# Performance work log

Hardware: AMD Instinct MI355X
Metric: run time of the kernel (lower is better)

## Reference

```python
import jax, jax.numpy as jnp
import numpy as np

NUM_HEADS = 8
H_NUM, W_NUM = 1, 2   # idx=0 stripe windows
SCALE = float((256 // NUM_HEADS) ** -0.5)  # qk_scale


def _partition(x, h_sp, w_sp):
    # x: (T,B,C,H,W) -> (T, B*nWin, heads, N, C//heads) with N = h_sp*w_sp
    T, B, C, H, W = x.shape
    x = x.reshape(T, B, C, H // h_sp, h_sp, W // w_sp, w_sp)
    x = x.transpose(0, 1, 3, 5, 4, 6, 2)  # T,B,nH,nW,h_sp,w_sp,C
    x = x.reshape(T, -1, h_sp * w_sp, NUM_HEADS, C // NUM_HEADS)
    return x.transpose(0, 1, 3, 2, 4)


def setup_inputs() -> dict:
    key = jax.random.key(0)
    k1, k2, k3 = jax.random.split(key, 3)
    shape = (4, 2, 256, 56, 56)
    return {
        "q": jax.random.normal(k1, shape, jnp.float32),
        "k": jax.random.normal(k2, shape, jnp.float32),
        "v": jax.random.normal(k3, shape, jnp.float32),
        "v_lamda": 1,
    }


def reference(q, k, v, v_lamda):
    T, B, C, H0, W0 = q.shape
    h_pad = (-H0) % H_NUM
    w_pad = (-W0) % W_NUM
    pad = ((0, 0), (0, 0), (0, 0), (0, h_pad), (0, w_pad))
    q = jnp.pad(q, pad)
    k = jnp.pad(k, pad)
    v = jnp.pad(v, pad)
    H, W = H0 + h_pad, W0 + w_pad
    h_sp, w_sp = H // H_NUM, W // W_NUM

    qw = _partition(q, h_sp, w_sp)  # (T, BnW, h, N, d)
    kw = _partition(k, h_sp, w_sp)
    vw = _partition(v, h_sp, w_sp)  # head dim = C*v_lamda//heads

    attn = jnp.einsum('twhnd,twhmd->twhnm', qw, kw)          # (QK^T), no softmax
    out = jnp.einsum('twhnm,twhmd->twhnd', attn, vw) * (SCALE * 2)

    # merge windows back: (T,BnW,h,N,d) -> (T,B,Cv,H,W)
    Cv = C * v_lamda
    out = out.transpose(0, 1, 3, 2, 4).reshape(T, -1, h_sp * w_sp, Cv)
    out = out.reshape(T, B, H_NUM, W_NUM, h_sp, w_sp, Cv)
    out = out.transpose(0, 1, 2, 4, 3, 5, 6).reshape(T, B, H, W, Cv)
    out = out.transpose(0, 1, 4, 2, 3)
    return out[:, :, :, :H0, :W0]
```

## Files before the change

### kernel.cpp

```cpp
#include <hip/hip_runtime.h>


#define HW 3136
#define WDIM 56
#define NPOS 1568
#define NPROB 128
#define SPLIT 14
#define PSPLIT 112
#define SCALE2 0.35355339059327373f

typedef const __attribute__((address_space(1))) void gas_void;
typedef __attribute__((address_space(3))) void las_void;

__global__ __launch_bounds__(256) void kv_kernel(const float* __restrict__ K,
                                                 const float* __restrict__ V,
                                                 float* __restrict__ Mpart) {
    __shared__ float lds[2 * 32 * PSPLIT];

    const int blk = blockIdx.x;
    const int p   = blk / SPLIT;
    const int s   = blk - p * SPLIT;
    const int head = p & 7;
    const int win  = (p >> 3) & 1;
    const int b    = (p >> 4) & 1;
    const int t    = p >> 5;

    const size_t base = (size_t)((t * 2 + b) * 256 + head * 32) * HW;
    const float* __restrict__ Kb = K + base;
    const float* __restrict__ Vb = V + base;

    const int tid = threadIdx.x;
    const int l   = tid & 63;
    const int w   = tid >> 6;

    #pragma unroll
    for (int i = 0; i < 7; ++i) {
        const int q   = (w * 7 + i) * 64 + l;
        const int isv = q >= 896 ? 1 : 0;
        const int r   = q - isv * 896;
        const int ch  = r / 28;
        const int pq  = r - ch * 28;
        const int n   = s * PSPLIT + pq * 4;
        const int y   = n / 28;
        const int x   = n - y * 28;
        const float* src = (isv ? Vb : Kb)
                         + (size_t)ch * HW + y * WDIM + win * 28 + x;
        float* dst = &lds[w * 1792 + i * 256];
        __builtin_amdgcn_global_load_lds((gas_void*)src, (las_void*)dst, 16, 0, 0);
    }
    __syncthreads();

    const int dd0 = (l >> 3) * 4;
    const int de0 = (l & 7) * 4;

    float acc[4][4] = {{0.f}};
    #pragma unroll
    for (int j = 0; j < 7; ++j) {
        const int n0 = 28 * w + 4 * j;
        float4 ka[4], va[4];
        #pragma unroll
        for (int i = 0; i < 4; ++i) {
            ka[i] = *(const float4*)&lds[(dd0 + i) * PSPLIT + n0];
            va[i] = *(const float4*)&lds[32 * PSPLIT + (de0 + i) * PSPLIT + n0];
        }
        #pragma unroll
        for (int i = 0; i < 4; ++i)
            #pragma unroll
            for (int jj = 0; jj < 4; ++jj)
                acc[i][jj] += ka[i].x * va[jj].x + ka[i].y * va[jj].y
                            + ka[i].z * va[jj].z + ka[i].w * va[jj].w;
    }
    __syncthreads();

    #pragma unroll
    for (int i = 0; i < 4; ++i)
        #pragma unroll
        for (int jj = 0; jj < 4; ++jj)
            lds[w * 1024 + (dd0 + i) * 32 + (de0 + jj)] = acc[i][jj];
    __syncthreads();

    const float4 r0 = *(const float4*)&lds[tid * 4];
    const float4 r1 = *(const float4*)&lds[1024 + tid * 4];
    const float4 r2 = *(const float4*)&lds[2048 + tid * 4];
    const float4 r3 = *(const float4*)&lds[3072 + tid * 4];
    float4 o;
    o.x = r0.x + r1.x + r2.x + r3.x;
    o.y = r0.y + r1.y + r2.y + r3.y;
    o.z = r0.z + r1.z + r2.z + r3.z;
    o.w = r0.w + r1.w + r2.w + r3.w;
    *(float4*)&Mpart[(size_t)blk * 1024 + tid * 4] = o;
}

__global__ __launch_bounds__(256) void qm_kernel(const float* __restrict__ Q,
                                                 const float* __restrict__ Mpart,
                                                 float* __restrict__ Out) {
    __shared__ float M[1024];
    const int blk = blockIdx.x;
    const int p   = blk / 7;
    const int c   = blk - p * 7;
    const int tid = threadIdx.x;

    const float* mp = Mpart + (size_t)p * SPLIT * 1024 + tid * 4;
    float4 sum = {0.f, 0.f, 0.f, 0.f};
    #pragma unroll
    for (int s = 0; s < SPLIT; ++s) {
        const float4 v = *(const float4*)&mp[s * 1024];
        sum.x += v.x; sum.y += v.y; sum.z += v.z; sum.w += v.w;
    }
    sum.x *= SCALE2; sum.y *= SCALE2; sum.z *= SCALE2; sum.w *= SCALE2;
    *(float4*)&M[tid * 4] = sum;
    __syncthreads();

    const int head = p & 7;
    const int win  = (p >> 3) & 1;
    const int b    = (p >> 4) & 1;
    const int t    = p >> 5;

    if (tid < 224) {
        const int n = c * 224 + tid;
        const int y = n / 28;
        const int x = n - y * 28;
        const size_t base = (size_t)((t * 2 + b) * 256 + head * 32) * HW
                          + y * WDIM + win * 28 + x;
        const float* __restrict__ Qb = Q + base;
        float* __restrict__ Ob = Out + base;

        float qv[32];
        #pragma unroll
        for (int dd = 0; dd < 32; ++dd)
            qv[dd] = Qb[(size_t)dd * HW];

        float acc[32] = {0.f};
        #pragma unroll 8
        for (int dd = 0; dd < 32; ++dd) {
            #pragma unroll
            for (int g = 0; g < 8; ++g) {
                const float4 m = *(const float4*)&M[dd * 32 + g * 4];
                acc[g * 4 + 0] += qv[dd] * m.x;
                acc[g * 4 + 1] += qv[dd] * m.y;
                acc[g * 4 + 2] += qv[dd] * m.z;
                acc[g * 4 + 3] += qv[dd] * m.w;
            }
        }
        #pragma unroll
        for (int de = 0; de < 32; ++de)
            Ob[(size_t)de * HW] = acc[de];
    }
}

extern "C" void kernel_launch(void* const* d_in, const int* in_sizes, int n_in,
                              void* d_out, int out_size, void* d_ws, size_t ws_size,
                              hipStream_t stream) {
    const float* q = (const float*)d_in[0];
    const float* k = (const float*)d_in[1];
    const float* v = (const float*)d_in[2];
    float* out   = (float*)d_out;
    float* Mpart = (float*)d_ws;

    kv_kernel<<<NPROB * SPLIT, 256, 0, stream>>>(k, v, Mpart);
    qm_kernel<<<NPROB * 7, 256, 0, stream>>>(q, Mpart, out);
}
```

Before: 135.5 us.

## Interleave K/V LDS layout and use packed FP32 FMA in both kernels

Changes the global-to-LDS staging in kv_kernel so each 4-position chunk stores 32 channels contiguously in a permuted order. This is meant to make the float4 LDS reads of K and V conflict-free. It also rewrites the inner products and the Q·M accumulation with 2-wide float vectors, so the compiler can emit packed FP32 FMA instructions. Accumulation order changes slightly, and more VGPRs may be needed.

```diff
diff --git a/kernel.cpp b/kernel.cpp
--- a/kernel.cpp
+++ b/kernel.cpp
@@ -3,7 +3,6 @@
 
 #define HW 3136
 #define WDIM 56
-#define NPOS 1568
 #define NPROB 128
 #define SPLIT 14
 #define PSPLIT 112
@@ -11,6 +10,7 @@
 
 typedef const __attribute__((address_space(1))) void gas_void;
 typedef __attribute__((address_space(3))) void las_void;
+typedef float v2f __attribute__((ext_vector_type(2)));
 
 __global__ __launch_bounds__(256) void kv_kernel(const float* __restrict__ K,
                                                  const float* __restrict__ V,
@@ -35,48 +35,57 @@
 
     #pragma unroll
     for (int i = 0; i < 7; ++i) {
-        const int q   = (w * 7 + i) * 64 + l;
-        const int isv = q >= 896 ? 1 : 0;
-        const int r   = q - isv * 896;
-        const int ch  = r / 28;
-        const int pq  = r - ch * 28;
-        const int n   = s * PSPLIT + pq * 4;
-        const int y   = n / 28;
-        const int x   = n - y * 28;
+        const int q    = (w * 7 + i) * 64 + l;
+        const int isv  = q >= 896 ? 1 : 0;
+        const int r    = q - isv * 896;
+        const int pq   = r >> 5;
+        const int slot = r & 31;
+        const int ch   = ((slot & 7) << 2) + (slot >> 3);
+        const int n    = s * PSPLIT + pq * 4;
+        const int y    = n / 28;
+        const int x    = n - y * 28;
         const float* src = (isv ? Vb : Kb)
                          + (size_t)ch * HW + y * WDIM + win * 28 + x;
-        float* dst = &lds[w * 1792 + i * 256];
+        float* dst = &lds[(w * 7 + i) * 256];
         __builtin_amdgcn_global_load_lds((gas_void*)src, (las_void*)dst, 16, 0, 0);
     }
     __syncthreads();
 
-    const int dd0 = (l >> 3) * 4;
-    const int de0 = (l & 7) * 4;
+    const int g = l >> 3;
+    const int e = l & 7;
 
-    float acc[4][4] = {{0.f}};
+    v2f acc2[4][4] = {};
     #pragma unroll
     for (int j = 0; j < 7; ++j) {
-        const int n0 = 28 * w + 4 * j;
+        const int rowb = (7 * w + j) * 128;
         float4 ka[4], va[4];
         #pragma unroll
         for (int i = 0; i < 4; ++i) {
-            ka[i] = *(const float4*)&lds[(dd0 + i) * PSPLIT + n0];
-            va[i] = *(const float4*)&lds[32 * PSPLIT + (de0 + i) * PSPLIT + n0];
+            ka[i] = *(const float4*)&lds[rowb + (g + 8 * i) * 4];
+            va[i] = *(const float4*)&lds[3584 + rowb + (e + 8 * i) * 4];
         }
         #pragma unroll
-        for (int i = 0; i < 4; ++i)
+        for (int i = 0; i < 4; ++i) {
+            const v2f ka_lo = {ka[i].x, ka[i].y};
+            const v2f ka_hi = {ka[i].z, ka[i].w};
             #pragma unroll
-            for (int jj = 0; jj < 4; ++jj)
-                acc[i][jj] += ka[i].x * va[jj].x + ka[i].y * va[jj].y
-                            + ka[i].z * va[jj].z + ka[i].w * va[jj].w;
+            for (int jj = 0; jj < 4; ++jj) {
+                const v2f va_lo = {va[jj].x, va[jj].y};
+                const v2f va_hi = {va[jj].z, va[jj].w};
+                acc2[i][jj] += ka_lo * va_lo;
+                acc2[i][jj] += ka_hi * va_hi;
+            }
+        }
     }
     __syncthreads();
 
+    const int dd0 = g * 4;
+    const int de0 = e * 4;
     #pragma unroll
     for (int i = 0; i < 4; ++i)
         #pragma unroll
         for (int jj = 0; jj < 4; ++jj)
-            lds[w * 1024 + (dd0 + i) * 32 + (de0 + jj)] = acc[i][jj];
+            lds[w * 1024 + (dd0 + i) * 32 + (de0 + jj)] = acc2[i][jj].x + acc2[i][jj].y;
     __syncthreads();
 
     const float4 r0 = *(const float4*)&lds[tid * 4];
@@ -101,13 +110,17 @@
     const int tid = threadIdx.x;
 
     const float* mp = Mpart + (size_t)p * SPLIT * 1024 + tid * 4;
-    float4 sum = {0.f, 0.f, 0.f, 0.f};
+    v2f s0 = {0.f, 0.f}, s1 = {0.f, 0.f};
     #pragma unroll
     for (int s = 0; s < SPLIT; ++s) {
         const float4 v = *(const float4*)&mp[s * 1024];
-        sum.x += v.x; sum.y += v.y; sum.z += v.z; sum.w += v.w;
+        const v2f vlo = {v.x, v.y};
+        const v2f vhi = {v.z, v.w};
+        s0 += vlo; s1 += vhi;
     }
-    sum.x *= SCALE2; sum.y *= SCALE2; sum.z *= SCALE2; sum.w *= SCALE2;
+    float4 sum;
+    sum.x = s0.x * SCALE2; sum.y = s0.y * SCALE2;
+    sum.z = s1.x * SCALE2; sum.w = s1.y * SCALE2;
     *(float4*)&M[tid * 4] = sum;
     __syncthreads();
 
@@ -130,21 +143,26 @@
         for (int dd = 0; dd < 32; ++dd)
             qv[dd] = Qb[(size_t)dd * HW];
 
-        float acc[32] = {0.f};
+        v2f acc2[16] = {};
         #pragma unroll 8
         for (int dd = 0; dd < 32; ++dd) {
+            const v2f qq = {qv[dd], qv[dd]};
             #pragma unroll
-            for (int g = 0; g < 8; ++g) {
-                const float4 m = *(const float4*)&M[dd * 32 + g * 4];
-                acc[g * 4 + 0] += qv[dd] * m.x;
-                acc[g * 4 + 1] += qv[dd] * m.y;
-                acc[g * 4 + 2] += qv[dd] * m.z;
-                acc[g * 4 + 3] += qv[dd] * m.w;
+            for (int gg = 0; gg < 8; ++gg) {
+                const float4 m = *(const float4*)&M[dd * 32 + gg * 4];
+                const v2f mlo = {m.x, m.y};
+                const v2f mhi = {m.z, m.w};
+                acc2[gg * 2 + 0] += qq * mlo;
+                acc2[gg * 2 + 1] += qq * mhi;
             }
         }
         #pragma unroll
-        for (int de = 0; de < 32; ++de)
-            Ob[(size_t)de * HW] = acc[de];
+        for (int gg = 0; gg < 8; ++gg) {
+            Ob[(size_t)(gg * 4 + 0) * HW] = acc2[gg * 2 + 0].x;
+            Ob[(size_t)(gg * 4 + 1) * HW] = acc2[gg * 2 + 0].y;
+            Ob[(size_t)(gg * 4 + 2) * HW] = acc2[gg * 2 + 1].x;
+            Ob[(size_t)(gg * 4 + 3) * HW] = acc2[gg * 2 + 1].y;
+        }
     }
 }
 
```

Result: faster. 129.2 us (-4.6%).
